# Performance work log

Hardware: AMD Instinct MI355X
Metric: run time of the kernel (lower is better)

## Reference

```python
import jax, jax.numpy as jnp
import numpy as np

IN, H, B = 256, 256, 65536


def setup_inputs() -> dict:
    key = jax.random.key(0)
    ks = jax.random.split(key, 20)
    s_in = 1.0 / np.sqrt(IN)
    s_h = 1.0 / np.sqrt(H)
    d = {
        "input": jax.random.normal(ks[0], (B, IN), jnp.float32),
        "hidden": jax.random.normal(ks[1], (B, H), jnp.float32),
        "cell": jax.random.normal(ks[2], (B, H), jnp.float32),
    }
    names_i = ["Wif", "Wii", "Wio", "Wig"]
    names_h = ["Whf", "Whi", "Who", "Whg"]
    for j, n in enumerate(names_i):
        d[n] = jax.random.uniform(ks[3 + j], (H, IN), jnp.float32, -s_in, s_in)
        d["b" + n[1:]] = jax.random.uniform(ks[7 + j], (H,), jnp.float32, -s_in, s_in)
    for j, n in enumerate(names_h):
        d[n] = jax.random.uniform(ks[11 + j], (H, H), jnp.float32, -s_h, s_h)
        d["b" + n[1:]] = jax.random.uniform(ks[15 + j], (H,), jnp.float32, -s_h, s_h)
    return d


def reference(input, hidden, cell,
              Wif, bif, Wii, bii, Wio, bio, Wig, big,
              Whf, bhf, Whi, bhi, Who, bho, Whg, bhg):
    # Fuse the 8 small linears into two [*,4H] GEMMs (same math as 8 separate Linear calls)
    Wi = jnp.concatenate([Wif, Wii, Wio, Wig], axis=0)  # [4H, IN]
    Wh = jnp.concatenate([Whf, Whi, Who, Whg], axis=0)  # [4H, H]
    bi = jnp.concatenate([bif, bii, bio, big])
    bh = jnp.concatenate([bhf, bhi, bho, bhg])
    gates = input @ Wi.T + bi + hidden @ Wh.T + bh  # [B, 4H]
    f, i, o, g = jnp.split(gates, 4, axis=1)
    f = jax.nn.sigmoid(f)
    i = jax.nn.sigmoid(i)
    o = jax.nn.sigmoid(o)
    g = jnp.tanh(g)
    new_cell = f * cell + i * g
    new_hidden = o * jnp.tanh(new_cell)
    output = jax.nn.log_softmax(new_hidden, axis=1)
    return output, new_hidden, new_cell
```

## Files before the change

### kernel.cpp

```cpp
#include <hip/hip_runtime.h>
#include <hip/hip_bf16.h>
#include <stdint.h>


#define BH 16777216

typedef float f32x4 __attribute__((ext_vector_type(4)));
typedef short short8 __attribute__((ext_vector_type(8)));

__device__ __forceinline__ unsigned short f2bf(float f) {
    union { float f; unsigned u; } v; v.f = f;
    unsigned u = v.u;
    return (unsigned short)((u + 0x7fffu + ((u >> 16) & 1u)) >> 16);
}

__device__ __forceinline__ unsigned pack2bf(float a, float b) {
    __hip_bfloat162 h = __float22bfloat162_rn(make_float2(a, b));
    union { __hip_bfloat162 h; unsigned u; } v; v.h = h;
    return v.u;
}

__device__ __forceinline__ float sigm(float x) { return 1.f / (1.f + __expf(-x)); }
__device__ __forceinline__ float tanh_(float x) { return 1.f - 2.f / (1.f + __expf(2.f * x)); }

__device__ __forceinline__ void glds16(const void* g, const void* l) {
    __builtin_amdgcn_global_load_lds(
        (const __attribute__((address_space(1))) unsigned int*)(uintptr_t)g,
        (__attribute__((address_space(3))) unsigned int*)(unsigned int)(uintptr_t)l,
        16, 0, 0);
}

__global__ __launch_bounds__(256) void pack_kernel(
    const float* __restrict__ Wif, const float* __restrict__ Wii,
    const float* __restrict__ Wio, const float* __restrict__ Wig,
    const float* __restrict__ Whf, const float* __restrict__ Whi,
    const float* __restrict__ Who, const float* __restrict__ Whg,
    const float* __restrict__ bif, const float* __restrict__ bii,
    const float* __restrict__ bio, const float* __restrict__ big,
    const float* __restrict__ bhf, const float* __restrict__ bhi,
    const float* __restrict__ bho, const float* __restrict__ bhg,
    unsigned short* __restrict__ wpack, float* __restrict__ bpack)
{
    const int t = blockIdx.x * 256 + threadIdx.x;
    const int n16  = t & 15;
    const int kg   = (t >> 4) & 3;
    const int Nt   = (t >> 6) & 15;
    const int step = (t >> 10) & 15;
    const int hg   = t >> 14;
    const int gate = Nt & 3;
    const int wc   = Nt >> 2;
    const int h    = hg * 64 + wc * 16 + n16;
    const int k0   = step * 32 + kg * 8;

    const float* Wi = (gate == 0) ? Wif : (gate == 1) ? Wii : (gate == 2) ? Wio : Wig;
    const float* Wh = (gate == 0) ? Whf : (gate == 1) ? Whi : (gate == 2) ? Who : Whg;
    const float* src = (k0 < 256) ? (Wi + h * 256 + k0) : (Wh + h * 256 + (k0 - 256));

    unsigned pk[4];
#pragma unroll
    for (int p = 0; p < 4; ++p)
        pk[p] = (unsigned)f2bf(src[p * 2]) | ((unsigned)f2bf(src[p * 2 + 1]) << 16);
    uint4 o4 = {pk[0], pk[1], pk[2], pk[3]};
    *(uint4*)&wpack[(size_t)t * 8] = o4;

    if (t < 1024) {
        const int cp = t;
        const int n2 = cp & 15, Nt2 = (cp >> 4) & 15, hg2 = cp >> 8;
        const int g2 = Nt2 & 3, wc2 = Nt2 >> 2;
        const int h2 = hg2 * 64 + wc2 * 16 + n2;
        const float* bi = (g2 == 0) ? bif : (g2 == 1) ? bii : (g2 == 2) ? bio : big;
        const float* bh = (g2 == 0) ? bhf : (g2 == 1) ? bhi : (g2 == 2) ? bho : bhg;
        bpack[cp] = bi[h2] + bh[h2];
    }
}

__global__ __launch_bounds__(512, 4) void lstm_gemm_kernel(
    const float* __restrict__ input, const float* __restrict__ hidden,
    const float* __restrict__ cell,
    const unsigned short* __restrict__ wpack, const float* __restrict__ bpack,
    float* __restrict__ out)
{
    __shared__ float Abuf[2][4096];
    __shared__ unsigned short Bbuf[2][8192];

    const int swz = (blockIdx.x & 7) * 256 + (blockIdx.x >> 3);
    const int hg    = swz & 3;
    const int panel = swz >> 2;
    const int row0  = panel * 128;

    const int tid = threadIdx.x;
    const int w = tid >> 6, l = tid & 63;
    const int wr = w >> 2, wc = w & 3;

    const int rowa  = tid >> 3;
    const int sA    = (tid & 7) ^ (rowa & 7);
    const size_t aoff0 = (size_t)(row0 + rowa) * 256 + sA * 4;
    const size_t aoff1 = aoff0 + (size_t)64 * 256;

    const unsigned short* wsrc = wpack + (size_t)hg * 131072 + w * 1024 + l * 8;

    glds16(input + aoff0, &Abuf[0][tid * 4]);
    glds16(input + aoff1, &Abuf[0][(tid + 512) * 4]);
    glds16(wsrc, &Bbuf[0][w * 1024]);
    glds16(wsrc + 512, &Bbuf[0][w * 1024 + 512]);
    __syncthreads();

    f32x4 acc[4][4] = {};

    const int r7  = l & 7;
    const int n16l = l & 15;
    const int kg2 = (l >> 4) * 2;

#pragma unroll 2
    for (int step = 0; step < 16; ++step) {
        const int cb = step & 1, nb = cb ^ 1;
        if (step < 15) {
            const int kn = (step + 1) * 32;
            const float* xb = (kn < 256) ? (input + kn) : (hidden + (kn - 256));
            glds16(xb + aoff0, &Abuf[nb][tid * 4]);
            glds16(xb + aoff1, &Abuf[nb][(tid + 512) * 4]);
            glds16(wsrc + (size_t)(step + 1) * 8192, &Bbuf[nb][w * 1024]);
            glds16(wsrc + (size_t)(step + 1) * 8192 + 512, &Bbuf[nb][w * 1024 + 512]);
        }
        short8 Af[4], Bf[4];
#pragma unroll
        for (int m = 0; m < 4; ++m) {
            const int row = wr * 64 + m * 16 + n16l;
            const int base = row * 32;
            float4 a0 = *(const float4*)&Abuf[cb][base + ((kg2    ) ^ r7) * 4];
            float4 a1 = *(const float4*)&Abuf[cb][base + ((kg2 + 1) ^ r7) * 4];
            union { uint4 u; short8 s; } cv;
            cv.u.x = pack2bf(a0.x, a0.y); cv.u.y = pack2bf(a0.z, a0.w);
            cv.u.z = pack2bf(a1.x, a1.y); cv.u.w = pack2bf(a1.z, a1.w);
            Af[m] = cv.s;
        }
#pragma unroll
        for (int n = 0; n < 4; ++n)
            Bf[n] = *(const short8*)&Bbuf[cb][((wc * 4 + n) * 64 + l) * 8];
#pragma unroll
        for (int m = 0; m < 4; ++m)
#pragma unroll
            for (int n = 0; n < 4; ++n)
                acc[m][n] = __builtin_amdgcn_mfma_f32_16x16x32_bf16(Af[m], Bf[n], acc[m][n], 0, 0, 0);
        __syncthreads();
    }

    const int lrow = l >> 4;
    const int hcol = hg * 64 + wc * 16 + n16l;
    float bias[4];
#pragma unroll
    for (int n = 0; n < 4; ++n)
        bias[n] = bpack[hg * 256 + wc * 64 + n * 16 + n16l];

#pragma unroll
    for (int m = 0; m < 4; ++m) {
#pragma unroll
        for (int rr = 0; rr < 4; ++rr) {
            const size_t rg_ = (size_t)row0 + wr * 64 + m * 16 + lrow * 4 + rr;
            const float fv = sigm(acc[m][0][rr] + bias[0]);
            const float iv = sigm(acc[m][1][rr] + bias[1]);
            const float ov = sigm(acc[m][2][rr] + bias[2]);
            const float gv = tanh_(acc[m][3][rr] + bias[3]);
            const float cv = cell[rg_ * 256 + hcol];
            const float nc = fv * cv + iv * gv;
            const float nhv = ov * tanh_(nc);
            out[(size_t)2 * BH + rg_ * 256 + hcol] = nc;
            out[(size_t)BH + rg_ * 256 + hcol] = nhv;
        }
    }
}

__global__ __launch_bounds__(256) void softmax_kernel(
    const float* __restrict__ nh, float* __restrict__ outp)
{
    const int w = threadIdx.x >> 6, l = threadIdx.x & 63;
#pragma unroll 1
    for (int it = 0; it < 8; ++it) {
        const size_t row = (size_t)it * 8192 + blockIdx.x * 4 + w;
        float4 v = *(const float4*)(nh + row * 256 + l * 4);
        float s = __expf(v.x) + __expf(v.y) + __expf(v.z) + __expf(v.w);
#pragma unroll
        for (int m = 1; m < 64; m <<= 1) s += __shfl_xor(s, m);
        const float lz = __logf(s);
        float4 o = {v.x - lz, v.y - lz, v.z - lz, v.w - lz};
        *(float4*)(outp + row * 256 + l * 4) = o;
    }
}

extern "C" void kernel_launch(void* const* d_in, const int* in_sizes, int n_in,
                              void* d_out, int out_size, void* d_ws, size_t ws_size,
                              hipStream_t stream)
{
    const float* input  = (const float*)d_in[0];
    const float* hidden = (const float*)d_in[1];
    const float* cell   = (const float*)d_in[2];
    const float* Wif = (const float*)d_in[3];  const float* bif = (const float*)d_in[4];
    const float* Wii = (const float*)d_in[5];  const float* bii = (const float*)d_in[6];
    const float* Wio = (const float*)d_in[7];  const float* bio = (const float*)d_in[8];
    const float* Wig = (const float*)d_in[9];  const float* big = (const float*)d_in[10];
    const float* Whf = (const float*)d_in[11]; const float* bhf = (const float*)d_in[12];
    const float* Whi = (const float*)d_in[13]; const float* bhi = (const float*)d_in[14];
    const float* Who = (const float*)d_in[15]; const float* bho = (const float*)d_in[16];
    const float* Whg = (const float*)d_in[17]; const float* bhg = (const float*)d_in[18];

    unsigned short* wpack = (unsigned short*)d_ws;
    float* bpack = (float*)((char*)d_ws + (size_t)1024 * 512 * 2);

    float* out = (float*)d_out;

    hipLaunchKernelGGL(pack_kernel, dim3(256), dim3(256), 0, stream,
        Wif, Wii, Wio, Wig, Whf, Whi, Who, Whg,
        bif, bii, bio, big, bhf, bhi, bho, bhg, wpack, bpack);

    hipLaunchKernelGGL(lstm_gemm_kernel, dim3(2048), dim3(512), 0, stream,
        input, hidden, cell, wpack, bpack, out);

    hipLaunchKernelGGL(softmax_kernel, dim3(2048), dim3(256), 0, stream,
        out + (size_t)BH, out);
}
```

Before: 176.8 us.

## Load A operand directly from global into registers, bypassing LDS staging

The A tiles (input/hidden activations) are no longer staged through a double-buffered LDS buffer. Each lane now loads its own float4 pairs straight from global memory into registers, prefetched one step ahead, and converts them to bf16 for the MFMA. This removes the LDS write and read traffic and frees 32KB of shared memory per block. In exchange, A rows are loaded redundantly by the four waves that share them and register pressure rises. s_setprio is also added around the MFMA block to favour the math waves.

```diff
diff --git a/kernel.cpp b/kernel.cpp
--- a/kernel.cpp
+++ b/kernel.cpp
@@ -80,7 +80,6 @@
     const unsigned short* __restrict__ wpack, const float* __restrict__ bpack,
     float* __restrict__ out)
 {
-    __shared__ float Abuf[2][4096];
     __shared__ unsigned short Bbuf[2][8192];
 
     const int swz = (blockIdx.x & 7) * 256 + (blockIdx.x >> 3);
@@ -91,57 +90,60 @@
     const int tid = threadIdx.x;
     const int w = tid >> 6, l = tid & 63;
     const int wr = w >> 2, wc = w & 3;
-
-    const int rowa  = tid >> 3;
-    const int sA    = (tid & 7) ^ (rowa & 7);
-    const size_t aoff0 = (size_t)(row0 + rowa) * 256 + sA * 4;
-    const size_t aoff1 = aoff0 + (size_t)64 * 256;
+    const int n16l = l & 15;
 
     const unsigned short* wsrc = wpack + (size_t)hg * 131072 + w * 1024 + l * 8;
 
-    glds16(input + aoff0, &Abuf[0][tid * 4]);
-    glds16(input + aoff1, &Abuf[0][(tid + 512) * 4]);
+    size_t arow[4];
+#pragma unroll
+    for (int m = 0; m < 4; ++m)
+        arow[m] = (size_t)(row0 + wr * 64 + m * 16 + n16l) * 256 + ((l >> 4) * 8);
+
     glds16(wsrc, &Bbuf[0][w * 1024]);
     glds16(wsrc + 512, &Bbuf[0][w * 1024 + 512]);
+    float4 a0[4], a1[4];
+#pragma unroll
+    for (int m = 0; m < 4; ++m) {
+        a0[m] = *(const float4*)(input + arow[m]);
+        a1[m] = *(const float4*)(input + arow[m] + 4);
+    }
     __syncthreads();
 
     f32x4 acc[4][4] = {};
-
-    const int r7  = l & 7;
-    const int n16l = l & 15;
-    const int kg2 = (l >> 4) * 2;
 
 #pragma unroll 2
     for (int step = 0; step < 16; ++step) {
         const int cb = step & 1, nb = cb ^ 1;
         if (step < 15) {
+            glds16(wsrc + (size_t)(step + 1) * 8192, &Bbuf[nb][w * 1024]);
+            glds16(wsrc + (size_t)(step + 1) * 8192 + 512, &Bbuf[nb][w * 1024 + 512]);
+        }
+        short8 Af[4];
+#pragma unroll
+        for (int m = 0; m < 4; ++m) {
+            union { uint4 u; short8 s; } cv;
+            cv.u.x = pack2bf(a0[m].x, a0[m].y); cv.u.y = pack2bf(a0[m].z, a0[m].w);
+            cv.u.z = pack2bf(a1[m].x, a1[m].y); cv.u.w = pack2bf(a1[m].z, a1[m].w);
+            Af[m] = cv.s;
+        }
+        if (step < 15) {
             const int kn = (step + 1) * 32;
             const float* xb = (kn < 256) ? (input + kn) : (hidden + (kn - 256));
-            glds16(xb + aoff0, &Abuf[nb][tid * 4]);
-            glds16(xb + aoff1, &Abuf[nb][(tid + 512) * 4]);
-            glds16(wsrc + (size_t)(step + 1) * 8192, &Bbuf[nb][w * 1024]);
-            glds16(wsrc + (size_t)(step + 1) * 8192 + 512, &Bbuf[nb][w * 1024 + 512]);
-        }
-        short8 Af[4], Bf[4];
-#pragma unroll
-        for (int m = 0; m < 4; ++m) {
-            const int row = wr * 64 + m * 16 + n16l;
-            const int base = row * 32;
-            float4 a0 = *(const float4*)&Abuf[cb][base + ((kg2    ) ^ r7) * 4];
-            float4 a1 = *(const float4*)&Abuf[cb][base + ((kg2 + 1) ^ r7) * 4];
-            union { uint4 u; short8 s; } cv;
-            cv.u.x = pack2bf(a0.x, a0.y); cv.u.y = pack2bf(a0.z, a0.w);
-            cv.u.z = pack2bf(a1.x, a1.y); cv.u.w = pack2bf(a1.z, a1.w);
-            Af[m] = cv.s;
-        }
-#pragma unroll
-        for (int n = 0; n < 4; ++n)
-            Bf[n] = *(const short8*)&Bbuf[cb][((wc * 4 + n) * 64 + l) * 8];
-#pragma unroll
-        for (int m = 0; m < 4; ++m)
-#pragma unroll
-            for (int n = 0; n < 4; ++n)
-                acc[m][n] = __builtin_amdgcn_mfma_f32_16x16x32_bf16(Af[m], Bf[n], acc[m][n], 0, 0, 0);
+#pragma unroll
+            for (int m = 0; m < 4; ++m) {
+                a0[m] = *(const float4*)(xb + arow[m]);
+                a1[m] = *(const float4*)(xb + arow[m] + 4);
+            }
+        }
+        __builtin_amdgcn_s_setprio(1);
+#pragma unroll
+        for (int n = 0; n < 4; ++n) {
+            short8 Bf = *(const short8*)&Bbuf[cb][(((wc * 4 + n) * 64 + l) << 3)];
+#pragma unroll
+            for (int m = 0; m < 4; ++m)
+                acc[m][n] = __builtin_amdgcn_mfma_f32_16x16x32_bf16(Af[m], Bf, acc[m][n], 0, 0, 0);
+        }
+        __builtin_amdgcn_s_setprio(0);
         __syncthreads();
     }
 
```

After: 449.2 us. 2.54x slower.
